# Performance work log

Hardware: AMD Instinct MI355X
Metric: run time of the kernel (lower is better)

The kernel has to match this reference:

```python
import jax, jax.numpy as jnp
import numpy as np

S = 0.1  # smoothing constant from __init__
EPS = 1e-08


def setup_inputs() -> dict:
    key = jax.random.key(0)
    am = jax.random.uniform(key, (64, 16, 65536), dtype=jnp.float32)
    return {"am": am}


def reference(am):
    B, K, N = am.shape
    # normalize each slot mask over pixels
    an = am / (jnp.sum(am, axis=-1, keepdims=True) + EPS)  # [B,K,N]
    sums = jnp.sum(an, axis=-1)  # [B,K]
    # pairwise intersections as one batched Gram matmul instead of K*(K-1)/2 tiny reductions
    gram = jnp.einsum('bkn,bln->bkl', an, an)  # [B,K,K]
    union = sums[:, :, None] + sums[:, None, :]  # [B,K,K]
    dice = (2.0 * gram + S) / (union + S)  # [B,K,K]
    per_pair = jnp.mean(dice, axis=0)  # [K,K], mean over batch per pair
    upper = jnp.triu(jnp.ones((K, K), dtype=bool), k=1)  # i < j pairs
    c = K * (K - 1) // 2
    total = jnp.sum(jnp.where(upper, per_pair, 0.0))
    return total / max(c, 1)
```

## Files before the change

kernel.cpp:

```cpp
#include <hip/hip_runtime.h>

#define B_ 64
#define K_ 16
#define N_ 65536
#define CHUNKS 16
#define CW (N_ / CHUNKS)
#define KB_PER_WAVE (CW / 32 / 4)
#define U_ 4
#define NGRP (KB_PER_WAVE / U_)
#define REC 272
#define NPAIR 120
#define EPS_ 1e-8f
#define SMOOTH_ 0.1f

typedef __attribute__((ext_vector_type(8))) short bf16x8;
typedef __attribute__((ext_vector_type(4))) float f32x4;

#define WS_REC_OFF 16

__device__ __forceinline__ short f2bf(float f) {
    unsigned u = __float_as_uint(f);
    return (short)((u + 0x7FFFu + ((u >> 16) & 1u)) >> 16);
}

template <int CTRL>
__device__ __forceinline__ float dpp_add_step(float x) {
    int y = __builtin_amdgcn_update_dpp(0, __float_as_int(x), CTRL, 0xf, 0xf, true);
    return x + __int_as_float(y);
}
__device__ __forceinline__ float wave_sum_lane63(float x) {
    x = dpp_add_step<0x111>(x);
    x = dpp_add_step<0x112>(x);
    x = dpp_add_step<0x114>(x);
    x = dpp_add_step<0x118>(x);
    x = dpp_add_step<0x142>(x);
    x = dpp_add_step<0x143>(x);
    return x;
}

__global__ __launch_bounds__(256, 4)
void dice_accum(const float* __restrict__ am, float* __restrict__ ws) {
    const int b     = blockIdx.x >> 4;
    const int chunk = blockIdx.x & (CHUNKS - 1);
    const int tid   = threadIdx.x;
    const int lane  = tid & 63;
    const int w     = tid >> 6;
    const int row   = lane & 15;
    const int lg    = lane >> 4;

    if (blockIdx.x == 0 && tid == 0) {
        reinterpret_cast<unsigned*>(ws)[0] = 0u;
        ws[1] = 0.f;
    }

    const f32x4* __restrict__ rp =
        reinterpret_cast<const f32x4*>(am)
        + (size_t)(b * K_ + row) * (N_ / 4)
        + chunk * (CW / 4)
        + lg * 2;

    const int rot = (b + chunk * 5 + w * 8) & (KB_PER_WAVE - 1);

    typedef __attribute__((ext_vector_type(4))) float accv;
    accv acc = {0.f, 0.f, 0.f, 0.f};
    float rs = 0.f;

    f32x4 aA[U_][2], aB[U_][2];

#define LOADG(dst, g) { _Pragma("unroll")                                     \
    for (int u = 0; u < U_; ++u) {                                            \
        const int kb = w + 4 * (((g) * U_ + u + rot) & (KB_PER_WAVE - 1));    \
        dst[u][0] = __builtin_nontemporal_load(&rp[kb * 8]);                  \
        dst[u][1] = __builtin_nontemporal_load(&rp[kb * 8 + 1]); } }

#define COMP(src) { _Pragma("unroll")                                         \
    for (int u = 0; u < U_; ++u) {                                            \
        const float f0 = src[u][0].x, f1 = src[u][0].y,                       \
                    f2 = src[u][0].z, f3 = src[u][0].w;                       \
        const float f4 = src[u][1].x, f5 = src[u][1].y,                       \
                    f6 = src[u][1].z, f7 = src[u][1].w;                       \
        rs += ((f0 + f1) + (f2 + f3)) + ((f4 + f5) + (f6 + f7));              \
        bf16x8 frag;                                                          \
        frag[0] = f2bf(f0); frag[1] = f2bf(f1);                               \
        frag[2] = f2bf(f2); frag[3] = f2bf(f3);                               \
        frag[4] = f2bf(f4); frag[5] = f2bf(f5);                               \
        frag[6] = f2bf(f6); frag[7] = f2bf(f7);                               \
        acc = __builtin_amdgcn_mfma_f32_16x16x32_bf16(frag, frag, acc, 0, 0, 0); } }

    LOADG(aA, 0)
#pragma unroll 1
    for (int g = 0; g < NGRP - 2; g += 2) {
        LOADG(aB, g + 1)
        COMP(aA)
        LOADG(aA, g + 2)
        COMP(aB)
    }
    LOADG(aB, NGRP - 1)
    COMP(aA)
    COMP(aB)
#undef LOADG
#undef COMP

    __shared__ float G_lds[4][256];
    __shared__ float RS_lds[4][64];
#pragma unroll
    for (int j = 0; j < 4; ++j)
        G_lds[w][(lg * 4 + j) * 16 + row] = acc[j];
    RS_lds[w][lane] = rs;
    __syncthreads();

    float* __restrict__ rec = ws + WS_REC_OFF + (size_t)blockIdx.x * REC;
    {
        float g = G_lds[0][tid] + G_lds[1][tid] + G_lds[2][tid] + G_lds[3][tid];
        rec[tid] = g;
    }
    if (tid < 16) {
        float s = 0.f;
#pragma unroll
        for (int ww = 0; ww < 4; ++ww)
#pragma unroll
            for (int g2 = 0; g2 < 4; ++g2) s += RS_lds[ww][g2 * 16 + tid];
        rec[256 + tid] = s;
    }
}

__global__ __launch_bounds__(256)
void dice_finalize(float* __restrict__ ws, float* __restrict__ out) {
    const int b   = blockIdx.x;
    const int tid = threadIdx.x;
    __shared__ float G[256];
    __shared__ float RS[16];
    __shared__ float red[128];
    __shared__ float bpart;

    const float* __restrict__ base = ws + WS_REC_OFF + (size_t)b * CHUNKS * REC;

    float g = 0.f;
#pragma unroll
    for (int r = 0; r < CHUNKS; ++r) g += base[r * REC + tid];
    G[tid] = g;
    if (tid < 16) {
        float s = 0.f;
#pragma unroll
        for (int r = 0; r < CHUNKS; ++r) s += base[r * REC + 256 + tid];
        RS[tid] = s;
    }
    __syncthreads();

    float acc = 0.f;
    if (tid < NPAIR) {
        int rem = tid, k = 0;
        while (rem >= K_ - 1 - k) { rem -= K_ - 1 - k; ++k; }
        const int l = k + 1 + rem;
        const float rsk = RS[k], rsl = RS[l];
        const float dk = rsk + EPS_, dl = rsl + EPS_;
        const float gram = G[k * 16 + l] / (dk * dl);
        const float u    = rsk / dk + rsl / dl;
        acc = (2.f * gram + SMOOTH_) / (u + SMOOTH_);
    }
    if (tid < 128) red[tid] = acc;
    __syncthreads();
    if (tid < 64) {
        float t = red[tid] + red[tid + 64];
        t = wave_sum_lane63(t);
        if (tid == 63) bpart = t;
    }
    __syncthreads();

    if (tid == 0) {
        atomicAdd(&ws[1], bpart);
        __threadfence();
        unsigned old = atomicAdd(reinterpret_cast<unsigned*>(ws), 1u);
        if (old == B_ - 1) {
            __threadfence();
            float total = __hip_atomic_load(&ws[1], __ATOMIC_RELAXED,
                                            __HIP_MEMORY_SCOPE_AGENT);
            out[0] = total / (float)(B_ * NPAIR);
        }
    }
}

extern "C" void kernel_launch(void* const* d_in, const int* in_sizes, int n_in,
                              void* d_out, int out_size, void* d_ws, size_t ws_size,
                              hipStream_t stream) {
    const float* am = (const float*)d_in[0];
    float* ws  = (float*)d_ws;
    float* out = (float*)d_out;

    hipLaunchKernelGGL(dice_accum, dim3(B_ * CHUNKS), dim3(256), 0, stream, am, ws);
    hipLaunchKernelGGL(dice_finalize, dim3(B_), dim3(256), 0, stream, ws, out);
}
```

Before: 56.81 us.

## Stage input through LDS with direct global-to-LDS loads and double buffering

Replaces per-thread register prefetching of the mask rows with direct global_load_lds transfers into a double-buffered 32KB shared-memory tile. A block-wide barrier separates each step, and an XOR swizzle is applied to avoid LDS bank conflicts when MFMA fragments are read back. The aim is to cut VGPR pressure and issue wider, more coalesced loads. In exchange it adds a __syncthreads per step, LDS read traffic, and a larger LDS footprint that may reduce occupancy.

```diff
diff --git a/kernel.cpp b/kernel.cpp
--- a/kernel.cpp
+++ b/kernel.cpp
@@ -1,13 +1,16 @@
 #include <hip/hip_runtime.h>
+#include <stdint.h>
 
 #define B_ 64
 #define K_ 16
 #define N_ 65536
 #define CHUNKS 16
 #define CW (N_ / CHUNKS)
-#define KB_PER_WAVE (CW / 32 / 4)
-#define U_ 4
-#define NGRP (KB_PER_WAVE / U_)
+#define STEPS 16
+#define SCOLS 256
+#define ROWB (SCOLS * 4)
+#define BUFB (K_ * ROWB)
+#define ROWSTRIDE ((size_t)N_ * 4)
 #define REC 272
 #define NPAIR 120
 #define EPS_ 1e-8f
@@ -17,6 +20,12 @@
 typedef __attribute__((ext_vector_type(4))) float f32x4;
 
 #define WS_REC_OFF 16
+
+typedef const __attribute__((address_space(1))) uint32_t* gas1_t;
+typedef __attribute__((address_space(3))) uint32_t*       las3_t;
+__device__ __forceinline__ void gload_lds16(const void* g, void* l) {
+    __builtin_amdgcn_global_load_lds((gas1_t)g, (las3_t)l, 16, 0, 0);
+}
 
 __device__ __forceinline__ short f2bf(float f) {
     unsigned u = __float_as_uint(f);
@@ -53,65 +62,67 @@
         ws[1] = 0.f;
     }
 
-    const f32x4* __restrict__ rp =
-        reinterpret_cast<const f32x4*>(am)
-        + (size_t)(b * K_ + row) * (N_ / 4)
-        + chunk * (CW / 4)
-        + lg * 2;
-
-    const int rot = (b + chunk * 5 + w * 8) & (KB_PER_WAVE - 1);
-
-    typedef __attribute__((ext_vector_type(4))) float accv;
-    accv acc = {0.f, 0.f, 0.f, 0.f};
+    __shared__ __align__(16) char smem[2 * BUFB];
+
+    const char* gbase = (const char*)am
+        + (size_t)(b * K_) * ROWSTRIDE + (size_t)chunk * (CW * 4);
+    const int rot = (b + chunk * 5) & (STEPS - 1);
+
+    f32x4 acc = {0.f, 0.f, 0.f, 0.f};
     float rs = 0.f;
-
-    f32x4 aA[U_][2], aB[U_][2];
-
-#define LOADG(dst, g) { _Pragma("unroll")                                     \
-    for (int u = 0; u < U_; ++u) {                                            \
-        const int kb = w + 4 * (((g) * U_ + u + rot) & (KB_PER_WAVE - 1));    \
-        dst[u][0] = __builtin_nontemporal_load(&rp[kb * 8]);                  \
-        dst[u][1] = __builtin_nontemporal_load(&rp[kb * 8 + 1]); } }
-
-#define COMP(src) { _Pragma("unroll")                                         \
-    for (int u = 0; u < U_; ++u) {                                            \
-        const float f0 = src[u][0].x, f1 = src[u][0].y,                       \
-                    f2 = src[u][0].z, f3 = src[u][0].w;                       \
-        const float f4 = src[u][1].x, f5 = src[u][1].y,                       \
-                    f6 = src[u][1].z, f7 = src[u][1].w;                       \
-        rs += ((f0 + f1) + (f2 + f3)) + ((f4 + f5) + (f6 + f7));              \
-        bf16x8 frag;                                                          \
-        frag[0] = f2bf(f0); frag[1] = f2bf(f1);                               \
-        frag[2] = f2bf(f2); frag[3] = f2bf(f3);                               \
-        frag[4] = f2bf(f4); frag[5] = f2bf(f5);                               \
-        frag[6] = f2bf(f6); frag[7] = f2bf(f7);                               \
-        acc = __builtin_amdgcn_mfma_f32_16x16x32_bf16(frag, frag, acc, 0, 0, 0); } }
-
-    LOADG(aA, 0)
+    const int xrd = (row >> 1) & 3;
+
+    auto stage = [&](int bi, int s) {
+        const size_t cs = (size_t)((s + rot) & (STEPS - 1)) * ROWB;
+#pragma unroll
+        for (int j = 0; j < 4; ++j) {
+            const int r  = w * 4 + j;
+            const int xr = (r >> 1) & 3;
+            const char* src = gbase + (size_t)r * ROWSTRIDE + cs
+                              + (size_t)((lane * 16) ^ (xr * 32));
+            gload_lds16(src, smem + bi * BUFB + r * ROWB);
+        }
+    };
+    auto compute = [&](int bi) {
+#pragma unroll
+        for (int t = 0; t < 2; ++t) {
+            const int kb = w + 4 * t;
+            const int p  = (kb * 4 + lg) ^ xrd;
+            const f32x4* q = (const f32x4*)(smem + bi * BUFB + row * ROWB + p * 32);
+            const f32x4 d0 = q[0];
+            const f32x4 d1 = q[1];
+            rs += ((d0.x + d0.y) + (d0.z + d0.w)) + ((d1.x + d1.y) + (d1.z + d1.w));
+            bf16x8 frag;
+            frag[0] = f2bf(d0.x); frag[1] = f2bf(d0.y);
+            frag[2] = f2bf(d0.z); frag[3] = f2bf(d0.w);
+            frag[4] = f2bf(d1.x); frag[5] = f2bf(d1.y);
+            frag[6] = f2bf(d1.z); frag[7] = f2bf(d1.w);
+            acc = __builtin_amdgcn_mfma_f32_16x16x32_bf16(frag, frag, acc, 0, 0, 0);
+        }
+    };
+
+    stage(0, 0);
+    __syncthreads();
 #pragma unroll 1
-    for (int g = 0; g < NGRP - 2; g += 2) {
-        LOADG(aB, g + 1)
-        COMP(aA)
-        LOADG(aA, g + 2)
-        COMP(aB)
-    }
-    LOADG(aB, NGRP - 1)
-    COMP(aA)
-    COMP(aB)
-#undef LOADG
-#undef COMP
-
-    __shared__ float G_lds[4][256];
-    __shared__ float RS_lds[4][64];
+    for (int s = 1; s < STEPS; ++s) {
+        stage(s & 1, s);
+        compute((s - 1) & 1);
+        __syncthreads();
+    }
+    compute((STEPS - 1) & 1);
+
+    float* G_lds  = (float*)smem;
+    float* RS_lds = (float*)(smem + 4096);
 #pragma unroll
     for (int j = 0; j < 4; ++j)
-        G_lds[w][(lg * 4 + j) * 16 + row] = acc[j];
-    RS_lds[w][lane] = rs;
+        G_lds[w * 256 + (lg * 4 + j) * 16 + row] = acc[j];
+    RS_lds[w * 64 + lane] = rs;
     __syncthreads();
 
     float* __restrict__ rec = ws + WS_REC_OFF + (size_t)blockIdx.x * REC;
     {
-        float g = G_lds[0][tid] + G_lds[1][tid] + G_lds[2][tid] + G_lds[3][tid];
+        float g = G_lds[0 * 256 + tid] + G_lds[1 * 256 + tid]
+                + G_lds[2 * 256 + tid] + G_lds[3 * 256 + tid];
         rec[tid] = g;
     }
     if (tid < 16) {
@@ -119,7 +130,7 @@
 #pragma unroll
         for (int ww = 0; ww < 4; ++ww)
 #pragma unroll
-            for (int g2 = 0; g2 < 4; ++g2) s += RS_lds[ww][g2 * 16 + tid];
+            for (int g2 = 0; g2 < 4; ++g2) s += RS_lds[ww * 64 + g2 * 16 + tid];
         rec[256 + tid] = s;
     }
 }
```

New measurement: 49.69 us. 1.14x faster.
